# Optimization experiments

Hardware: AMD Instinct MI355X
Metric: run time of the kernel (lower is better)

Reference implementation:

```python
import jax, jax.numpy as jnp
import numpy as np

VOCAB, D, H, S, L = 50257, 512, 1024, 2048, 16
TWO_H = 2 * H


def setup_inputs() -> dict:
    key = jax.random.key(0)
    ks = jax.random.split(key, 20)
    sc = 0.02
    return {
        "token": jax.random.randint(ks[0], (1,), 0, VOCAB),
        "hidden": jax.random.normal(ks[1], (1, 1, H), jnp.float32),
        "encoder_outputs": jax.random.normal(ks[2], (S, TWO_H), jnp.float32),
        "nlg_class": jax.random.uniform(ks[3], (L,), jnp.float32),
        "embedding": jax.random.normal(ks[4], (VOCAB, D), jnp.float32) * sc,
        "attn_W": jax.random.normal(ks[5], (H, TWO_H), jnp.float32) * sc,
        "attn_b": jnp.zeros((H,), jnp.float32),
        "comb_W": jax.random.normal(ks[6], (H, D + TWO_H + L), jnp.float32) * sc,
        "comb_b": jnp.zeros((H,), jnp.float32),
        "fc1_W": jax.random.normal(ks[7], (H, H), jnp.float32) * sc,
        "fc1_b": jnp.zeros((H,), jnp.float32),
        "fc2_W": jax.random.normal(ks[8], (H, H), jnp.float32) * sc,
        "fc2_b": jnp.zeros((H,), jnp.float32),
        "gru_Wih": jax.random.normal(ks[9], (3 * H, H), jnp.float32) * sc,
        "gru_Whh": jax.random.normal(ks[10], (3 * H, H), jnp.float32) * sc,
        "gru_bih": jnp.zeros((3 * H,), jnp.float32),
        "gru_bhh": jnp.zeros((3 * H,), jnp.float32),
        "out_W": jax.random.normal(ks[11], (VOCAB, H + L + D), jnp.float32) * sc,
        "out_b": jnp.zeros((VOCAB,), jnp.float32),
    }


def reference(token, hidden, encoder_outputs, nlg_class, embedding,
              attn_W, attn_b, comb_W, comb_b, fc1_W, fc1_b, fc2_W, fc2_b,
              gru_Wih, gru_Whh, gru_bih, gru_bhh, out_W, out_b):
    # Single decode step, batch=1. Dropout is identity (eval mode).
    emb = embedding[token].reshape(1, -1)               # [1, D]
    h_flat = hidden.reshape(-1)                          # [H]

    # Bahdanau-style attention: vectorized replacement of the per-timestep loop
    energy = encoder_outputs @ attn_W.T + attn_b         # [S, H]
    scores = jax.nn.softmax(energy @ h_flat)             # [S]
    attn_weights = scores.reshape(1, 1, -1)              # [1,1,S]
    context = scores[None, :] @ encoder_outputs          # [1, 2H]

    x = jnp.concatenate([emb, context, nlg_class[None, :]], axis=1)
    x = jax.nn.relu(x @ comb_W.T + comb_b)
    x = jax.nn.relu(x @ fc1_W.T + fc1_b)
    x = jax.nn.relu(x @ fc2_W.T + fc2_b)                 # [1, H]

    # One GRU step (PyTorch gate ordering r,z,n)
    h_prev = hidden[0]                                   # [1, H]
    gi = x @ gru_Wih.T + gru_bih                         # [1, 3H]
    gh = h_prev @ gru_Whh.T + gru_bhh                    # [1, 3H]
    i_r, i_z, i_n = jnp.split(gi, 3, axis=1)
    h_r, h_z, h_n = jnp.split(gh, 3, axis=1)
    r = jax.nn.sigmoid(i_r + h_r)
    z = jax.nn.sigmoid(i_z + h_z)
    n = jnp.tanh(i_n + r * h_n)
    h_new = (1.0 - z) * n + z * h_prev                   # [1, H]

    logits = jnp.concatenate([h_new, nlg_class[None, :], emb], axis=1) @ out_W.T + out_b
    out = jax.nn.log_softmax(logits, axis=1)             # [1, VOCAB]
    return out, h_new.reshape(1, 1, -1), attn_weights
```

## Files before the change

kernel.cpp:

```cpp
#include <hip/hip_runtime.h>
#include <hip/hip_bf16.h>
#include <math.h>

#define VOCAB 50257
#define DD 512
#define H 1024
#define SS 2048
#define LL 16
#define TWO_H 2048
#define XDIM 2576
#define YDIM 1552

#define OFF_V      0
#define OFF_CTX    2048
#define OFF_RAW    4096
#define OFF_SC     6144
#define OFF_X1     8192
#define OFF_X2     9216
#define OFF_X3     10240
#define OFF_G      11264
#define OFF_Y      17408
#define OFF_LOGITS 18960
#define OFF_PSUM   69220
#define OFF_GMAXU  69348

__device__ __forceinline__ float bf2f(unsigned short s) {
  union { unsigned u; float f; } t; t.u = ((unsigned)s) << 16; return t.f;
}
__device__ __forceinline__ float bflo(unsigned w) {
  union { unsigned u; float f; } t; t.u = w << 16; return t.f;
}
__device__ __forceinline__ float bfhi(unsigned w) {
  union { unsigned u; float f; } t; t.u = w & 0xffff0000u; return t.f;
}
__device__ __forceinline__ unsigned short f2bf(float f) {
  union { float f; unsigned u; } t; t.f = f;
  unsigned r = (t.u + 0x7FFFu + ((t.u >> 16) & 1u)) >> 16;
  return (unsigned short)r;
}
template<bool BF>
__device__ __forceinline__ float ldv(const void* p, size_t i) {
  if (BF) return bf2f(((const unsigned short*)p)[i]);
  else    return ((const float*)p)[i];
}
template<bool BF>
__device__ __forceinline__ void stv(void* p, size_t i, float v) {
  if (BF) ((unsigned short*)p)[i] = f2bf(v);
  else    ((float*)p)[i] = v;
}

__device__ __forceinline__ unsigned enc_f(float f) {
  unsigned u = __float_as_uint(f);
  return (u & 0x80000000u) ? ~u : (u | 0x80000000u);
}
__device__ __forceinline__ float dec_f(unsigned u) {
  unsigned v = (u & 0x80000000u) ? (u & 0x7FFFFFFFu) : ~u;
  return __uint_as_float(v);
}

__device__ __forceinline__ float block_reduce_256(float acc) {
  #pragma unroll
  for (int off = 32; off; off >>= 1) acc += __shfl_down(acc, off, 64);
  __shared__ float r4[4];
  if ((threadIdx.x & 63) == 0) r4[threadIdx.x >> 6] = acc;
  __syncthreads();
  return r4[0] + r4[1] + r4[2] + r4[3];
}

template<bool BF>
__global__ __launch_bounds__(256)
void init_kernel(const void* __restrict__ nlg, const void* __restrict__ embedding,
                 const int* __restrict__ token, float* __restrict__ ws) {
  int i = blockIdx.x * 256 + threadIdx.x;
  if (i < 4096) ws[OFF_V + i] = 0.f;
  if (i == 4100) *(unsigned*)(ws + OFF_GMAXU) = 0u;
  int j = i - 4352;
  if (j >= 0 && j < (YDIM - H)) {
    float v;
    if (j < LL) v = ldv<BF>(nlg, j);
    else        v = ldv<BF>(embedding, (size_t)token[0] * DD + (j - LL));
    ws[OFF_Y + H + j] = v;
  }
}

template<bool BF>
__global__ __launch_bounds__(256)
void attn_v_kernel(const void* __restrict__ W, const void* __restrict__ hidden,
                   float* __restrict__ v) {
  __shared__ float hs[32];
  int j0 = blockIdx.y * 32;
  if (threadIdx.x < 32) hs[threadIdx.x] = ldv<BF>(hidden, j0 + threadIdx.x);
  __syncthreads();
  int k = blockIdx.x * 256 + threadIdx.x;
  float acc = 0.f;
  #pragma unroll 8
  for (int j = 0; j < 32; ++j)
    acc += ldv<BF>(W, (size_t)(j0 + j) * TWO_H + k) * hs[j];
  atomicAdd(&v[k], acc);
}

template<bool BF, bool RELU>
__global__ __launch_bounds__(256)
void matvec_kernel(const void* __restrict__ W, const void* __restrict__ bias,
                   const float* __restrict__ x, float* __restrict__ out, int K) {
  int row = blockIdx.x, t = threadIdx.x;
  float acc = 0.f;
  int nc = K >> 2;
  if (BF) {
    const uint2* Wr = (const uint2*)((const unsigned short*)W + (size_t)row * K);
    for (int c = t; c < nc; c += 256) {
      uint2 u = Wr[c]; const float* xp = x + c * 4;
      acc += bflo(u.x)*xp[0] + bfhi(u.x)*xp[1] + bflo(u.y)*xp[2] + bfhi(u.y)*xp[3];
    }
  } else {
    const float4* Wr = (const float4*)((const float*)W + (size_t)row * K);
    for (int c = t; c < nc; c += 256) {
      float4 u = Wr[c]; const float* xp = x + c * 4;
      acc += u.x*xp[0] + u.y*xp[1] + u.z*xp[2] + u.w*xp[3];
    }
  }
  float s = block_reduce_256(acc);
  if (t == 0) {
    if (bias) s += ldv<BF>(bias, row);
    if (RELU) s = fmaxf(s, 0.f);
    out[row] = s;
  }
}

template<bool BF>
__global__ __launch_bounds__(256)
void softmax2048_kernel(const float* __restrict__ raw, float* __restrict__ scores,
                        void* __restrict__ d_out) {
  __shared__ float red[256];
  int t = threadIdx.x;
  float m = -3.4e38f;
  for (int i = t; i < SS; i += 256) m = fmaxf(m, raw[i]);
  red[t] = m; __syncthreads();
  for (int s = 128; s; s >>= 1) { if (t < s) red[t] = fmaxf(red[t], red[t + s]); __syncthreads(); }
  float gm = red[0]; __syncthreads();
  float sum = 0.f;
  for (int i = t; i < SS; i += 256) { float e = expf(raw[i] - gm); scores[i] = e; sum += e; }
  red[t] = sum; __syncthreads();
  for (int s = 128; s; s >>= 1) { if (t < s) red[t] += red[t + s]; __syncthreads(); }
  float inv = 1.f / red[0];
  for (int i = t; i < SS; i += 256) {
    float sc = scores[i] * inv;
    scores[i] = sc;
    stv<BF>(d_out, (size_t)(VOCAB + H) + i, sc);
  }
}

template<bool BF>
__global__ __launch_bounds__(256)
void context_kernel(const void* __restrict__ enc, const float* __restrict__ scores,
                    float* __restrict__ ctx) {
  __shared__ float ss[64];
  int s0 = blockIdx.y * 64;
  if (threadIdx.x < 64) ss[threadIdx.x] = scores[s0 + threadIdx.x];
  __syncthreads();
  int k = blockIdx.x * 256 + threadIdx.x;
  float acc = 0.f;
  #pragma unroll 8
  for (int s = 0; s < 64; ++s)
    acc += ss[s] * ldv<BF>(enc, (size_t)(s0 + s) * TWO_H + k);
  atomicAdd(&ctx[k], acc);
}

template<bool BF>
__global__ __launch_bounds__(256)
void comb_kernel(const void* __restrict__ W, const void* __restrict__ bias,
                 const void* __restrict__ embedding, const float* __restrict__ ctx,
                 const void* __restrict__ nlg, const int* __restrict__ token,
                 float* __restrict__ out) {
  int row = blockIdx.x, t = threadIdx.x;
  size_t ebase = (size_t)token[0] * DD;
  float acc = 0.f;
  for (int c4 = t; c4 < (XDIM >> 2); c4 += 256) {
    int c = c4 << 2;
    float x0, x1, x2, x3v;
    if (c < DD) {
      x0 = ldv<BF>(embedding, ebase + c);     x1 = ldv<BF>(embedding, ebase + c + 1);
      x2 = ldv<BF>(embedding, ebase + c + 2); x3v = ldv<BF>(embedding, ebase + c + 3);
    } else if (c < DD + TWO_H) {
      const float* cp = ctx + (c - DD);
      x0 = cp[0]; x1 = cp[1]; x2 = cp[2]; x3v = cp[3];
    } else {
      int b = c - DD - TWO_H;
      x0 = ldv<BF>(nlg, b);     x1 = ldv<BF>(nlg, b + 1);
      x2 = ldv<BF>(nlg, b + 2); x3v = ldv<BF>(nlg, b + 3);
    }
    if (BF) {
      uint2 u = ((const uint2*)((const unsigned short*)W + (size_t)row * XDIM))[c4];
      acc += bflo(u.x)*x0 + bfhi(u.x)*x1 + bflo(u.y)*x2 + bfhi(u.y)*x3v;
    } else {
      float4 u = ((const float4*)((const float*)W + (size_t)row * XDIM))[c4];
      acc += u.x*x0 + u.y*x1 + u.z*x2 + u.w*x3v;
    }
  }
  float s = block_reduce_256(acc);
  if (t == 0) out[row] = fmaxf(s + ldv<BF>(bias, row), 0.f);
}

template<bool BF>
__global__ __launch_bounds__(256)
void gru2_kernel(const void* __restrict__ Wih, const void* __restrict__ Whh,
                 const void* __restrict__ bih, const void* __restrict__ bhh,
                 const float* __restrict__ x3, const void* __restrict__ hidden,
                 float* __restrict__ g) {
  int row = blockIdx.x, t = threadIdx.x;
  bool ih = row < 3 * H;
  int r = ih ? row : row - 3 * H;
  const void* W = ih ? Wih : Whh;
  float x0, x1, x2, x3v;
  if (ih) {
    const float* xp = x3 + t * 4;
    x0 = xp[0]; x1 = xp[1]; x2 = xp[2]; x3v = xp[3];
  } else {
    x0 = ldv<BF>(hidden, 4 * t);     x1 = ldv<BF>(hidden, 4 * t + 1);
    x2 = ldv<BF>(hidden, 4 * t + 2); x3v = ldv<BF>(hidden, 4 * t + 3);
  }
  float acc;
  if (BF) {
    uint2 u = ((const uint2*)((const unsigned short*)W + (size_t)r * H))[t];
    acc = bflo(u.x)*x0 + bfhi(u.x)*x1 + bflo(u.y)*x2 + bfhi(u.y)*x3v;
  } else {
    float4 u = ((const float4*)((const float*)W + (size_t)r * H))[t];
    acc = u.x*x0 + u.y*x1 + u.z*x2 + u.w*x3v;
  }
  float s = block_reduce_256(acc);
  if (t == 0) g[row] = s + ldv<BF>(ih ? bih : bhh, r);
}

template<bool BF>
__global__ __launch_bounds__(256)
void gates_kernel(const float* __restrict__ g, const void* __restrict__ hidden,
                  float* __restrict__ y, void* __restrict__ d_out) {
  int i = blockIdx.x * 256 + threadIdx.x;
  if (i >= H) return;
  const float* gi = g;
  const float* gh = g + 3 * H;
  float r = 1.f / (1.f + expf(-(gi[i] + gh[i])));
  float z = 1.f / (1.f + expf(-(gi[H + i] + gh[H + i])));
  float n = tanhf(gi[2 * H + i] + r * gh[2 * H + i]);
  float hp = ldv<BF>(hidden, i);
  float hn = (1.f - z) * n + z * hp;
  y[i] = hn;
  stv<BF>(d_out, (size_t)VOCAB + i, hn);
}

template<bool BF>
__global__ __launch_bounds__(512)
void logits_kernel(const void* __restrict__ W, const void* __restrict__ bias,
                   const float* __restrict__ y, float* __restrict__ logits,
                   unsigned* __restrict__ gmaxU) {
  __shared__ float ys[YDIM];
  for (int i = threadIdx.x; i < YDIM; i += 512) ys[i] = y[i];
  __syncthreads();
  int wave = threadIdx.x >> 6, lane = threadIdx.x & 63;
  int row = blockIdx.x * 8 + wave;
  float val = -3.4e38f;
  if (row < VOCAB) {
    float acc = 0.f;
    if (BF) {
      const unsigned short* Wr = (const unsigned short*)W + (size_t)row * YDIM;
      for (int c = lane; c < (YDIM >> 3); c += 64) {
        uint4 u = ((const uint4*)Wr)[c];
        const float* xp = ys + (c << 3);
        acc += bflo(u.x)*xp[0] + bfhi(u.x)*xp[1] + bflo(u.y)*xp[2] + bfhi(u.y)*xp[3]
             + bflo(u.z)*xp[4] + bfhi(u.z)*xp[5] + bflo(u.w)*xp[6] + bfhi(u.w)*xp[7];
      }
    } else {
      const float* Wr = (const float*)W + (size_t)row * YDIM;
      for (int c = lane; c < (YDIM >> 2); c += 64) {
        float4 u = ((const float4*)Wr)[c];
        const float* xp = ys + (c << 2);
        acc += u.x*xp[0] + u.y*xp[1] + u.z*xp[2] + u.w*xp[3];
      }
    }
    #pragma unroll
    for (int off = 32; off; off >>= 1) acc += __shfl_down(acc, off, 64);
    if (lane == 0) {
      float lv = acc + ldv<BF>(bias, row);
      logits[row] = lv;
      val = lv;
    }
  }
  __shared__ float wmax[8];
  if (lane == 0) wmax[wave] = val;
  __syncthreads();
  if (threadIdx.x == 0) {
    float m = wmax[0];
    #pragma unroll
    for (int k = 1; k < 8; ++k) m = fmaxf(m, wmax[k]);
    atomicMax(gmaxU, enc_f(m));
  }
}

__global__ __launch_bounds__(256)
void psum_kernel(const float* __restrict__ logits, const unsigned* __restrict__ gmaxU,
                 float* __restrict__ psum) {
  float gm = dec_f(*gmaxU);
  float s = 0.f;
  for (int i = blockIdx.x * 256 + threadIdx.x; i < VOCAB; i += 128 * 256)
    s += expf(logits[i] - gm);
  float tot = block_reduce_256(s);
  if (threadIdx.x == 0) psum[blockIdx.x] = tot;
}

template<bool BF>
__global__ __launch_bounds__(256)
void writeout_kernel(const float* __restrict__ logits, const float* __restrict__ psum,
                     const unsigned* __restrict__ gmaxU, void* __restrict__ out) {
  int t = threadIdx.x;
  float s = (t < 128) ? psum[t] : 0.f;
  float tot = block_reduce_256(s);
  __shared__ float lz;
  if (t == 0) lz = dec_f(*gmaxU) + logf(tot);
  __syncthreads();
  int i = blockIdx.x * 256 + t;
  if (i < VOCAB) stv<BF>(out, i, logits[i] - lz);
}

template<bool BF>
static void launch_all(void* const* d_in, void* d_out, float* ws, hipStream_t stream) {
  const int* token      = (const int*)d_in[0];
  const void* hidden    = d_in[1];
  const void* enc       = d_in[2];
  const void* nlg       = d_in[3];
  const void* embedding = d_in[4];
  const void* attn_W    = d_in[5];
  const void* comb_W    = d_in[7];
  const void* comb_b    = d_in[8];
  const void* fc1_W     = d_in[9];
  const void* fc1_b     = d_in[10];
  const void* fc2_W     = d_in[11];
  const void* fc2_b     = d_in[12];
  const void* gru_Wih   = d_in[13];
  const void* gru_Whh   = d_in[14];
  const void* gru_bih   = d_in[15];
  const void* gru_bhh   = d_in[16];
  const void* out_W     = d_in[17];
  const void* out_b     = d_in[18];

  unsigned* gmaxU = (unsigned*)(ws + OFF_GMAXU);

  init_kernel<BF><<<20, 256, 0, stream>>>(nlg, embedding, token, ws);
  attn_v_kernel<BF><<<dim3(8, 32), 256, 0, stream>>>(attn_W, hidden, ws + OFF_V);
  matvec_kernel<BF, false><<<SS, 256, 0, stream>>>(enc, nullptr, ws + OFF_V, ws + OFF_RAW, TWO_H);
  softmax2048_kernel<BF><<<1, 256, 0, stream>>>(ws + OFF_RAW, ws + OFF_SC, d_out);
  context_kernel<BF><<<dim3(8, 32), 256, 0, stream>>>(enc, ws + OFF_SC, ws + OFF_CTX);
  comb_kernel<BF><<<H, 256, 0, stream>>>(comb_W, comb_b, embedding, ws + OFF_CTX, nlg, token, ws + OFF_X1);
  matvec_kernel<BF, true><<<H, 256, 0, stream>>>(fc1_W, fc1_b, ws + OFF_X1, ws + OFF_X2, H);
  matvec_kernel<BF, true><<<H, 256, 0, stream>>>(fc2_W, fc2_b, ws + OFF_X2, ws + OFF_X3, H);
  gru2_kernel<BF><<<6 * H, 256, 0, stream>>>(gru_Wih, gru_Whh, gru_bih, gru_bhh,
                                             ws + OFF_X3, hidden, ws + OFF_G);
  gates_kernel<BF><<<4, 256, 0, stream>>>(ws + OFF_G, hidden, ws + OFF_Y, d_out);
  logits_kernel<BF><<<(VOCAB + 7) / 8, 512, 0, stream>>>(out_W, out_b, ws + OFF_Y,
                                                         ws + OFF_LOGITS, gmaxU);
  psum_kernel<<<128, 256, 0, stream>>>(ws + OFF_LOGITS, gmaxU, ws + OFF_PSUM);
  writeout_kernel<BF><<<(VOCAB + 255) / 256, 256, 0, stream>>>(ws + OFF_LOGITS, ws + OFF_PSUM,
                                                               gmaxU, d_out);
}

extern "C" void kernel_launch(void* const* d_in, const int* in_sizes, int n_in,
                              void* d_out, int out_size, void* d_ws, size_t ws_size,
                              hipStream_t stream) {
  (void)n_in; (void)out_size; (void)ws_size;
  bool bf = (in_sizes && in_sizes[4] == VOCAB * DD * 2);
  float* ws = (float*)d_ws;
  if (bf) launch_all<true >(d_in, d_out, ws, stream);
  else    launch_all<false>(d_in, d_out, ws, stream);
}
```

Measured before the change: 575.1 us.

## Fuse all decode stages into one cooperative persistent kernel with grid syncs

Replaces the chain of thirteen kernel launches with a single cooperative kernel of 1024 blocks that runs every stage (attention, MLP, GRU, logits, log-softmax) and separates them with grid-wide barriers. This removes per-launch overhead and the gaps between dependent kernels. The final log-softmax is restructured into per-block max and sum partials. The trade-off is a fixed grid size, which reduces parallelism in the large logits matvec, and many grid.sync barriers. The old multi-kernel path is kept as a fallback if the cooperative launch fails.

```diff
diff --git a/kernel.cpp b/kernel.cpp
--- a/kernel.cpp
+++ b/kernel.cpp
@@ -1,6 +1,8 @@
 #include <hip/hip_runtime.h>
-#include <hip/hip_bf16.h>
+#include <hip/hip_cooperative_groups.h>
 #include <math.h>
+
+namespace cg = cooperative_groups;
 
 #define VOCAB 50257
 #define DD 512
@@ -10,6 +12,7 @@
 #define TWO_H 2048
 #define XDIM 2576
 #define YDIM 1552
+#define NB 1024
 
 #define OFF_V      0
 #define OFF_CTX    2048
@@ -21,8 +24,10 @@
 #define OFF_G      11264
 #define OFF_Y      17408
 #define OFF_LOGITS 18960
-#define OFF_PSUM   69220
-#define OFF_GMAXU  69348
+#define OFF_PMAX   69220
+#define OFF_PSUMP  70244
+#define OFF_FBPSUM 71268
+#define OFF_GMAXU  71396
 
 __device__ __forceinline__ float bf2f(unsigned short s) {
   union { unsigned u; float f; } t; t.u = ((unsigned)s) << 16; return t.f;
@@ -48,7 +53,6 @@
   if (BF) ((unsigned short*)p)[i] = f2bf(v);
   else    ((float*)p)[i] = v;
 }
-
 __device__ __forceinline__ unsigned enc_f(float f) {
   unsigned u = __float_as_uint(f);
   return (u & 0x80000000u) ? ~u : (u | 0x80000000u);
@@ -56,6 +60,311 @@
 __device__ __forceinline__ float dec_f(unsigned u) {
   unsigned v = (u & 0x80000000u) ? (u & 0x7FFFFFFFu) : ~u;
   return __uint_as_float(v);
+}
+
+__device__ __forceinline__ float wave_reduce(float acc) {
+  #pragma unroll
+  for (int off = 32; off; off >>= 1) acc += __shfl_down(acc, off, 64);
+  return acc;
+}
+__device__ __forceinline__ float wave_allreduce(float acc) {
+  #pragma unroll
+  for (int off = 32; off; off >>= 1) acc += __shfl_xor(acc, off, 64);
+  return acc;
+}
+__device__ __forceinline__ float wave_allreduce_max(float m) {
+  #pragma unroll
+  for (int off = 32; off; off >>= 1) m = fmaxf(m, __shfl_xor(m, off, 64));
+  return m;
+}
+
+template<bool BF>
+__global__ __launch_bounds__(256, 4)
+void mega_kernel(const int* __restrict__ token,
+                 const void* __restrict__ hidden,
+                 const void* __restrict__ enc,
+                 const void* __restrict__ nlg,
+                 const void* __restrict__ embedding,
+                 const void* __restrict__ attn_W,
+                 const void* __restrict__ comb_W, const void* __restrict__ comb_b,
+                 const void* __restrict__ fc1_W, const void* __restrict__ fc1_b,
+                 const void* __restrict__ fc2_W, const void* __restrict__ fc2_b,
+                 const void* __restrict__ gru_Wih, const void* __restrict__ gru_Whh,
+                 const void* __restrict__ gru_bih, const void* __restrict__ gru_bhh,
+                 const void* __restrict__ out_W, const void* __restrict__ out_b,
+                 float* __restrict__ ws, void* __restrict__ d_out) {
+  cg::grid_group grid = cg::this_grid();
+  const int bid = blockIdx.x, t = threadIdx.x;
+  const int wave = t >> 6, lane = t & 63;
+  const int gw = bid * 4 + wave;
+  const int gid = bid * 256 + t;
+
+  __shared__ float ys[YDIM];
+  __shared__ float sred[256];
+  __shared__ float hs[32];
+  __shared__ float scs[64];
+
+  if (gid < 4096) ws[OFF_V + gid] = 0.f;
+  {
+    int j = gid - 4352;
+    if (j >= 0 && j < (LL + DD)) {
+      float v = (j < LL) ? ldv<BF>(nlg, j)
+                         : ldv<BF>(embedding, (size_t)token[0] * DD + (j - LL));
+      ws[OFF_Y + H + j] = v;
+    }
+  }
+  grid.sync();
+
+  if (bid < 256) {
+    int kblk = bid & 7, jblk = bid >> 3;
+    int j0 = jblk * 32;
+    if (t < 32) hs[t] = ldv<BF>(hidden, j0 + t);
+    __syncthreads();
+    int k = kblk * 256 + t;
+    float acc = 0.f;
+    #pragma unroll 8
+    for (int jj = 0; jj < 32; ++jj)
+      acc += ldv<BF>(attn_W, (size_t)(j0 + jj) * TWO_H + k) * hs[jj];
+    atomicAdd(&ws[OFF_V + k], acc);
+  }
+  grid.sync();
+
+  if (gw < SS) {
+    const float* vv = ws + OFF_V;
+    float acc = 0.f;
+    if (BF) {
+      const uint4* Er = (const uint4*)((const unsigned short*)enc + (size_t)gw * TWO_H);
+      #pragma unroll 4
+      for (int c = lane; c < (TWO_H >> 3); c += 64) {
+        uint4 u = Er[c]; const float* xp = vv + (c << 3);
+        acc += bflo(u.x)*xp[0] + bfhi(u.x)*xp[1] + bflo(u.y)*xp[2] + bfhi(u.y)*xp[3]
+             + bflo(u.z)*xp[4] + bfhi(u.z)*xp[5] + bflo(u.w)*xp[6] + bfhi(u.w)*xp[7];
+      }
+    } else {
+      const float4* Er = (const float4*)((const float*)enc + (size_t)gw * TWO_H);
+      #pragma unroll 4
+      for (int c = lane; c < (TWO_H >> 2); c += 64) {
+        float4 u = Er[c]; const float* xp = vv + (c << 2);
+        acc += u.x*xp[0] + u.y*xp[1] + u.z*xp[2] + u.w*xp[3];
+      }
+    }
+    acc = wave_reduce(acc);
+    if (lane == 0) ws[OFF_RAW + gw] = acc;
+  }
+  grid.sync();
+
+  if (bid == 0) {
+    float m = -3.4e38f;
+    for (int i = t; i < SS; i += 256) m = fmaxf(m, ws[OFF_RAW + i]);
+    sred[t] = m; __syncthreads();
+    for (int s = 128; s; s >>= 1) { if (t < s) sred[t] = fmaxf(sred[t], sred[t + s]); __syncthreads(); }
+    float gm = sred[0]; __syncthreads();
+    float sum = 0.f;
+    for (int i = t; i < SS; i += 256) { float e = expf(ws[OFF_RAW + i] - gm); ws[OFF_SC + i] = e; sum += e; }
+    sred[t] = sum; __syncthreads();
+    for (int s = 128; s; s >>= 1) { if (t < s) sred[t] += sred[t + s]; __syncthreads(); }
+    float inv = 1.f / sred[0];
+    for (int i = t; i < SS; i += 256) {
+      float sc = ws[OFF_SC + i] * inv;
+      ws[OFF_SC + i] = sc;
+      stv<BF>(d_out, (size_t)(VOCAB + H) + i, sc);
+    }
+  }
+  grid.sync();
+
+  if (bid < 256) {
+    int kblk = bid & 7, sblk = bid >> 3;
+    int s0 = sblk * 64;
+    if (t < 64) scs[t] = ws[OFF_SC + s0 + t];
+    __syncthreads();
+    int k = kblk * 256 + t;
+    float acc = 0.f;
+    #pragma unroll 8
+    for (int s = 0; s < 64; ++s)
+      acc += scs[s] * ldv<BF>(enc, (size_t)(s0 + s) * TWO_H + k);
+    atomicAdd(&ws[OFF_CTX + k], acc);
+  }
+  grid.sync();
+
+  {
+    int row = bid;
+    size_t ebase = (size_t)token[0] * DD;
+    float acc = 0.f;
+    for (int c4 = t; c4 < (XDIM >> 2); c4 += 256) {
+      int c = c4 << 2;
+      float x0, x1, x2, x3v;
+      if (c < DD) {
+        x0 = ldv<BF>(embedding, ebase + c);     x1 = ldv<BF>(embedding, ebase + c + 1);
+        x2 = ldv<BF>(embedding, ebase + c + 2); x3v = ldv<BF>(embedding, ebase + c + 3);
+      } else if (c < DD + TWO_H) {
+        const float* cp = ws + OFF_CTX + (c - DD);
+        x0 = cp[0]; x1 = cp[1]; x2 = cp[2]; x3v = cp[3];
+      } else {
+        int b = c - DD - TWO_H;
+        x0 = ldv<BF>(nlg, b);     x1 = ldv<BF>(nlg, b + 1);
+        x2 = ldv<BF>(nlg, b + 2); x3v = ldv<BF>(nlg, b + 3);
+      }
+      if (BF) {
+        uint2 u = ((const uint2*)((const unsigned short*)comb_W + (size_t)row * XDIM))[c4];
+        acc += bflo(u.x)*x0 + bfhi(u.x)*x1 + bflo(u.y)*x2 + bfhi(u.y)*x3v;
+      } else {
+        float4 u = ((const float4*)((const float*)comb_W + (size_t)row * XDIM))[c4];
+        acc += u.x*x0 + u.y*x1 + u.z*x2 + u.w*x3v;
+      }
+    }
+    acc = wave_reduce(acc);
+    if (lane == 0) sred[wave] = acc;
+    __syncthreads();
+    if (t == 0)
+      ws[OFF_X1 + row] = fmaxf(sred[0] + sred[1] + sred[2] + sred[3] + ldv<BF>(comb_b, row), 0.f);
+  }
+  grid.sync();
+
+  {
+    int row = bid;
+    const float* xp = ws + OFF_X1 + t * 4;
+    float acc;
+    if (BF) {
+      uint2 u = ((const uint2*)((const unsigned short*)fc1_W + (size_t)row * H))[t];
+      acc = bflo(u.x)*xp[0] + bfhi(u.x)*xp[1] + bflo(u.y)*xp[2] + bfhi(u.y)*xp[3];
+    } else {
+      float4 u = ((const float4*)((const float*)fc1_W + (size_t)row * H))[t];
+      acc = u.x*xp[0] + u.y*xp[1] + u.z*xp[2] + u.w*xp[3];
+    }
+    acc = wave_reduce(acc);
+    if (lane == 0) sred[wave] = acc;
+    __syncthreads();
+    if (t == 0)
+      ws[OFF_X2 + row] = fmaxf(sred[0] + sred[1] + sred[2] + sred[3] + ldv<BF>(fc1_b, row), 0.f);
+  }
+  grid.sync();
+
+  {
+    int row = bid;
+    const float* xp = ws + OFF_X2 + t * 4;
+    float acc;
+    if (BF) {
+      uint2 u = ((const uint2*)((const unsigned short*)fc2_W + (size_t)row * H))[t];
+      acc = bflo(u.x)*xp[0] + bfhi(u.x)*xp[1] + bflo(u.y)*xp[2] + bfhi(u.y)*xp[3];
+    } else {
+      float4 u = ((const float4*)((const float*)fc2_W + (size_t)row * H))[t];
+      acc = u.x*xp[0] + u.y*xp[1] + u.z*xp[2] + u.w*xp[3];
+    }
+    acc = wave_reduce(acc);
+    if (lane == 0) sred[wave] = acc;
+    __syncthreads();
+    if (t == 0)
+      ws[OFF_X3 + row] = fmaxf(sred[0] + sred[1] + sred[2] + sred[3] + ldv<BF>(fc2_b, row), 0.f);
+  }
+  grid.sync();
+
+  for (int rr = gw; rr < 6 * H; rr += 4096) {
+    bool ih = rr < 3 * H;
+    int r = ih ? rr : rr - 3 * H;
+    const void* W = ih ? gru_Wih : gru_Whh;
+    float acc = 0.f;
+    #pragma unroll
+    for (int p = 0; p < 4; ++p) {
+      int c4 = lane + p * 64;
+      float x0, x1, x2, x3v;
+      if (ih) {
+        const float* xp = ws + OFF_X3 + c4 * 4;
+        x0 = xp[0]; x1 = xp[1]; x2 = xp[2]; x3v = xp[3];
+      } else {
+        x0 = ldv<BF>(hidden, c4 * 4);     x1 = ldv<BF>(hidden, c4 * 4 + 1);
+        x2 = ldv<BF>(hidden, c4 * 4 + 2); x3v = ldv<BF>(hidden, c4 * 4 + 3);
+      }
+      if (BF) {
+        uint2 u = ((const uint2*)((const unsigned short*)W + (size_t)r * H))[c4];
+        acc += bflo(u.x)*x0 + bfhi(u.x)*x1 + bflo(u.y)*x2 + bfhi(u.y)*x3v;
+      } else {
+        float4 u = ((const float4*)((const float*)W + (size_t)r * H))[c4];
+        acc += u.x*x0 + u.y*x1 + u.z*x2 + u.w*x3v;
+      }
+    }
+    acc = wave_reduce(acc);
+    if (lane == 0) ws[OFF_G + rr] = acc + ldv<BF>(ih ? gru_bih : gru_bhh, r);
+  }
+  grid.sync();
+
+  if (gid < H) {
+    const float* gi = ws + OFF_G;
+    const float* gh = ws + OFF_G + 3 * H;
+    int i = gid;
+    float r = 1.f / (1.f + expf(-(gi[i] + gh[i])));
+    float z = 1.f / (1.f + expf(-(gi[H + i] + gh[H + i])));
+    float n = tanhf(gi[2 * H + i] + r * gh[2 * H + i]);
+    float hp = ldv<BF>(hidden, i);
+    float hn = (1.f - z) * n + z * hp;
+    ws[OFF_Y + i] = hn;
+    stv<BF>(d_out, (size_t)VOCAB + i, hn);
+  }
+  grid.sync();
+
+  for (int i = t; i < YDIM; i += 256) ys[i] = ws[OFF_Y + i];
+  __syncthreads();
+  {
+    float wmax = -3.4e38f;
+    for (int row = gw; row < VOCAB; row += 4096) {
+      float acc = 0.f;
+      if (BF) {
+        const unsigned short* Wr = (const unsigned short*)out_W + (size_t)row * YDIM;
+        for (int c = lane; c < (YDIM >> 3); c += 64) {
+          uint4 u = ((const uint4*)Wr)[c];
+          const float* xp = ys + (c << 3);
+          acc += bflo(u.x)*xp[0] + bfhi(u.x)*xp[1] + bflo(u.y)*xp[2] + bfhi(u.y)*xp[3]
+               + bflo(u.z)*xp[4] + bfhi(u.z)*xp[5] + bflo(u.w)*xp[6] + bfhi(u.w)*xp[7];
+        }
+      } else {
+        const float* Wr = (const float*)out_W + (size_t)row * YDIM;
+        for (int c = lane; c < (YDIM >> 2); c += 64) {
+          float4 u = ((const float4*)Wr)[c];
+          const float* xp = ys + (c << 2);
+          acc += u.x*xp[0] + u.y*xp[1] + u.z*xp[2] + u.w*xp[3];
+        }
+      }
+      acc = wave_reduce(acc);
+      if (lane == 0) {
+        float lv = acc + ldv<BF>(out_b, row);
+        ws[OFF_LOGITS + row] = lv;
+        wmax = fmaxf(wmax, lv);
+      }
+    }
+    if (lane == 0) sred[wave] = wmax;
+    __syncthreads();
+    if (t == 0)
+      ws[OFF_PMAX + bid] = fmaxf(fmaxf(sred[0], sred[1]), fmaxf(sred[2], sred[3]));
+  }
+  grid.sync();
+
+  float gm_save;
+  {
+    float m = fmaxf(fmaxf(ws[OFF_PMAX + t], ws[OFF_PMAX + t + 256]),
+                    fmaxf(ws[OFF_PMAX + t + 512], ws[OFF_PMAX + t + 768]));
+    m = wave_allreduce_max(m);
+    if (lane == 0) sred[wave] = m;
+    __syncthreads();
+    float gm = fmaxf(fmaxf(sred[0], sred[1]), fmaxf(sred[2], sred[3]));
+    __syncthreads();
+    gm_save = gm;
+    float s = (gid < VOCAB) ? expf(ws[OFF_LOGITS + gid] - gm) : 0.f;
+    s = wave_allreduce(s);
+    if (lane == 0) sred[wave] = s;
+    __syncthreads();
+    if (t == 0) ws[OFF_PSUMP + bid] = sred[0] + sred[1] + sred[2] + sred[3];
+  }
+  grid.sync();
+
+  {
+    float s = ws[OFF_PSUMP + t] + ws[OFF_PSUMP + t + 256]
+            + ws[OFF_PSUMP + t + 512] + ws[OFF_PSUMP + t + 768];
+    s = wave_allreduce(s);
+    if (lane == 0) sred[wave] = s;
+    __syncthreads();
+    float tot = sred[0] + sred[1] + sred[2] + sred[3];
+    float lz = gm_save + logf(tot);
+    if (gid < VOCAB) stv<BF>(d_out, gid, ws[OFF_LOGITS + gid] - lz);
+  }
 }
 
 __device__ __forceinline__ float block_reduce_256(float acc) {
@@ -253,8 +562,8 @@
 void logits_kernel(const void* __restrict__ W, const void* __restrict__ bias,
                    const float* __restrict__ y, float* __restrict__ logits,
                    unsigned* __restrict__ gmaxU) {
-  __shared__ float ys[YDIM];
-  for (int i = threadIdx.x; i < YDIM; i += 512) ys[i] = y[i];
+  __shared__ float ysl[YDIM];
+  for (int i = threadIdx.x; i < YDIM; i += 512) ysl[i] = y[i];
   __syncthreads();
   int wave = threadIdx.x >> 6, lane = threadIdx.x & 63;
   int row = blockIdx.x * 8 + wave;
@@ -265,7 +574,7 @@
       const unsigned short* Wr = (const unsigned short*)W + (size_t)row * YDIM;
       for (int c = lane; c < (YDIM >> 3); c += 64) {
         uint4 u = ((const uint4*)Wr)[c];
-        const float* xp = ys + (c << 3);
+        const float* xp = ysl + (c << 3);
         acc += bflo(u.x)*xp[0] + bfhi(u.x)*xp[1] + bflo(u.y)*xp[2] + bfhi(u.y)*xp[3]
              + bflo(u.z)*xp[4] + bfhi(u.z)*xp[5] + bflo(u.w)*xp[6] + bfhi(u.w)*xp[7];
       }
@@ -273,7 +582,7 @@
       const float* Wr = (const float*)W + (size_t)row * YDIM;
       for (int c = lane; c < (YDIM >> 2); c += 64) {
         float4 u = ((const float4*)Wr)[c];
-        const float* xp = ys + (c << 2);
+        const float* xp = ysl + (c << 2);
         acc += u.x*xp[0] + u.y*xp[1] + u.z*xp[2] + u.w*xp[3];
       }
     }
@@ -322,7 +631,7 @@
 }
 
 template<bool BF>
-static void launch_all(void* const* d_in, void* d_out, float* ws, hipStream_t stream) {
+static void launch_fallback(void* const* d_in, void* d_out, float* ws, hipStream_t stream) {
   const int* token      = (const int*)d_in[0];
   const void* hidden    = d_in[1];
   const void* enc       = d_in[2];
@@ -341,7 +650,6 @@
   const void* gru_bhh   = d_in[16];
   const void* out_W     = d_in[17];
   const void* out_b     = d_in[18];
-
   unsigned* gmaxU = (unsigned*)(ws + OFF_GMAXU);
 
   init_kernel<BF><<<20, 256, 0, stream>>>(nlg, embedding, token, ws);
@@ -357,9 +665,41 @@
   gates_kernel<BF><<<4, 256, 0, stream>>>(ws + OFF_G, hidden, ws + OFF_Y, d_out);
   logits_kernel<BF><<<(VOCAB + 7) / 8, 512, 0, stream>>>(out_W, out_b, ws + OFF_Y,
                                                          ws + OFF_LOGITS, gmaxU);
-  psum_kernel<<<128, 256, 0, stream>>>(ws + OFF_LOGITS, gmaxU, ws + OFF_PSUM);
-  writeout_kernel<BF><<<(VOCAB + 255) / 256, 256, 0, stream>>>(ws + OFF_LOGITS, ws + OFF_PSUM,
+  psum_kernel<<<128, 256, 0, stream>>>(ws + OFF_LOGITS, gmaxU, ws + OFF_FBPSUM);
+  writeout_kernel<BF><<<(VOCAB + 255) / 256, 256, 0, stream>>>(ws + OFF_LOGITS, ws + OFF_FBPSUM,
                                                                gmaxU, d_out);
+}
+
+template<bool BF>
+static void launch_mega(void* const* d_in, void* d_out, float* ws, hipStream_t stream) {
+  const int* token      = (const int*)d_in[0];
+  const void* hidden    = d_in[1];
+  const void* enc       = d_in[2];
+  const void* nlg       = d_in[3];
+  const void* embedding = d_in[4];
+  const void* attn_W    = d_in[5];
+  const void* comb_W    = d_in[7];
+  const void* comb_b    = d_in[8];
+  const void* fc1_W     = d_in[9];
+  const void* fc1_b     = d_in[10];
+  const void* fc2_W     = d_in[11];
+  const void* fc2_b     = d_in[12];
+  const void* gru_Wih   = d_in[13];
+  const void* gru_Whh   = d_in[14];
+  const void* gru_bih   = d_in[15];
+  const void* gru_bhh   = d_in[16];
+  const void* out_W     = d_in[17];
+  const void* out_b     = d_in[18];
+  void* outp = d_out;
+  float* wsp = ws;
+
+  void* args[] = { &token, &hidden, &enc, &nlg, &embedding, &attn_W,
+                   &comb_W, &comb_b, &fc1_W, &fc1_b, &fc2_W, &fc2_b,
+                   &gru_Wih, &gru_Whh, &gru_bih, &gru_bhh, &out_W, &out_b,
+                   &wsp, &outp };
+  hipError_t e = hipLaunchCooperativeKernel((const void*)mega_kernel<BF>,
+                                            dim3(NB), dim3(256), args, 0, stream);
+  if (e != hipSuccess) launch_fallback<BF>(d_in, d_out, ws, stream);
 }
 
 extern "C" void kernel_launch(void* const* d_in, const int* in_sizes, int n_in,
@@ -368,6 +708,6 @@
   (void)n_in; (void)out_size; (void)ws_size;
   bool bf = (in_sizes && in_sizes[4] == VOCAB * DD * 2);
   float* ws = (float*)d_ws;
-  if (bf) launch_all<true >(d_in, d_out, ws, stream);
-  else    launch_all<false>(d_in, d_out, ws, stream);
-}
+  if (bf) launch_mega<true >(d_in, d_out, ws, stream);
+  else    launch_mega<false>(d_in, d_out, ws, stream);
+}
```

Measured after the change: 1.814 ms. 3.15x slower.
